# Kernel tuning notes

Hardware: AMD Instinct MI355X
Metric: run time of the kernel (lower is better)

The kernel has to match this reference:

```python
import jax, jax.numpy as jnp
import numpy as np

L, H, NH, NKV, HD, I, V, B, S = 18, 640, 4, 1, 256, 2048, 32768, 1, 1024
WINDOW = 512
EPS = 1e-6
THETA_G = 1000000.0
THETA_L = 10000.0


def _rms(x, w):
    # Gemma RMSNorm: x / rms(x) * (1 + w)
    var = jnp.mean(jnp.square(x), axis=-1, keepdims=True)
    return x * jax.lax.rsqrt(var + EPS) * (1.0 + w)


def _rope_tables(theta):
    inv = 1.0 / (theta ** (jnp.arange(0, HD, 2, dtype=jnp.float32) / HD))
    f = jnp.arange(S, dtype=jnp.float32)[:, None] * inv[None, :]
    emb = jnp.concatenate([f, f], axis=-1)  # [S, HD]
    return jnp.cos(emb), jnp.sin(emb)


def _rope(x, cos, sin):
    # x: [B, S, n, HD]
    x1, x2 = jnp.split(x, 2, axis=-1)
    rot = jnp.concatenate([-x2, x1], axis=-1)
    return x * cos[None, :, None, :] + rot * sin[None, :, None, :]


def setup_inputs() -> dict:
    key = jax.random.key(0)
    ks = jax.random.split(key, 16)
    r = lambda k, sh: jax.random.normal(k, sh, jnp.float32) * 0.02
    return {
        'input_ids': jax.random.randint(ks[0], (B, S), 0, V, jnp.int32),
        'is_full': jnp.array([(i + 1) % 6 == 0 for i in range(L)]),
        'embed': r(ks[1], (V, H)),
        'wq': r(ks[2], (L, H, NH * HD)),
        'wk': r(ks[3], (L, H, NKV * HD)),
        'wv': r(ks[4], (L, H, NKV * HD)),
        'wo': r(ks[5], (L, NH * HD, H)),
        'qn': jnp.zeros((L, HD)), 'kn': jnp.zeros((L, HD)),
        'ln1': jnp.zeros((L, H)), 'ln2': jnp.zeros((L, H)),
        'ln3': jnp.zeros((L, H)), 'ln4': jnp.zeros((L, H)),
        'wg': r(ks[6], (L, H, I)), 'wu': r(ks[7], (L, H, I)),
        'wd': r(ks[8], (L, I, H)),
        'norm_w': jnp.zeros((H,)),
    }


def _forward(embed, wq, wk, wv, wo, qn, kn, ln1, ln2, ln3, ln4, wg, wu, wd,
             norm_w, input_ids, is_full):
    cos_g, sin_g = _rope_tables(THETA_G)
    cos_l, sin_l = _rope_tables(THETA_L)
    pos = jnp.arange(S)
    causal = pos[:, None] >= pos[None, :]
    sliding = causal & ((pos[:, None] - pos[None, :]) < WINDOW)
    scale = HD ** -0.5
    grp = NH // NKV

    h = embed[input_ids] * jnp.asarray(H ** 0.5, embed.dtype)  # [B,S,H]

    def body(h, xs):
        (wq_, wk_, wv_, wo_, qn_, kn_, l1, l2, l3, l4, wg_, wu_, wd_, full) = xs
        cos = jnp.where(full, cos_g, cos_l)
        sin = jnp.where(full, sin_g, sin_l)
        mask = jnp.where(full, causal, sliding)
        x = _rms(h, l1)
        q = (x @ wq_).reshape(B, S, NH, HD)
        k = (x @ wk_).reshape(B, S, NKV, HD)
        v = (x @ wv_).reshape(B, S, NKV, HD)
        q = _rope(_rms(q, qn_), cos, sin)
        k = _rope(_rms(k, kn_), cos, sin)
        qg = q.reshape(B, S, NKV, grp, HD)
        scores = jnp.einsum('bqngd,bsnd->bngqs', qg, k) * scale
        scores = jnp.where(mask[None, None, None], scores, -1e30)
        attn = jax.nn.softmax(scores, axis=-1)
        o = jnp.einsum('bngqs,bsnd->bqngd', attn, v).reshape(B, S, NH * HD)
        h = h + _rms(o @ wo_, l2)               # post_attention_layernorm then residual
        x = _rms(h, l3)                          # pre_feedforward_layernorm
        mlp = (jax.nn.gelu(x @ wg_, approximate=True) * (x @ wu_)) @ wd_  # GeGLU
        h = h + _rms(mlp, l4)                    # post_feedforward_layernorm then residual
        return h, None

    h, _ = jax.lax.scan(body, h, (wq, wk, wv, wo, qn, kn, ln1, ln2, ln3, ln4, wg, wu, wd, is_full))
    h = _rms(h, norm_w)
    # lm_head tied to embed_tokens; final_logit_softcapping = 0.0 (disabled)
    return jnp.einsum('bsh,vh->bsv', h, embed)


def reference(input_ids, is_full, embed, wq, wk, wv, wo, qn, kn,
              ln1, ln2, ln3, ln4, wg, wu, wd, norm_w):
    return _forward(embed, wq, wk, wv, wo, qn, kn, ln1, ln2, ln3, ln4,
                    wg, wu, wd, norm_w, input_ids, is_full)
```

## Files before the change

kernel.cpp:

```cpp
#include <hip/hip_runtime.h>


typedef unsigned short u16;
typedef __attribute__((ext_vector_type(4))) float f32x4;
typedef __attribute__((ext_vector_type(8))) short bf16x8;

#define DEV static __device__ __forceinline__

DEV u16 f2bf(float f) {
  union { float f; unsigned u; } x; x.f = f;
  unsigned r = x.u + 0x7fffu + ((x.u >> 16) & 1u);
  return (u16)(r >> 16);
}

#define GLOAD16(gp, lp) __builtin_amdgcn_global_load_lds( \
    (const __attribute__((address_space(1))) void*)(gp), \
    (__attribute__((address_space(3))) void*)(lp), 16, 0, 0)

DEV float blockSum(float v, float* red) {
#pragma unroll
  for (int o = 32; o; o >>= 1) v += __shfl_down(v, o);
  int lane = threadIdx.x & 63, wid = threadIdx.x >> 6;
  if (lane == 0) red[wid] = v;
  __syncthreads();
  float s = red[0] + red[1] + red[2] + red[3];
  __syncthreads();
  return s;
}

DEV float blockMax(float v, float* red) {
#pragma unroll
  for (int o = 32; o; o >>= 1) v = fmaxf(v, __shfl_down(v, o));
  int lane = threadIdx.x & 63, wid = threadIdx.x >> 6;
  if (lane == 0) red[wid] = v;
  __syncthreads();
  float s = fmaxf(fmaxf(red[0], red[1]), fmaxf(red[2], red[3]));
  __syncthreads();
  return s;
}

DEV void cstore(float* C, size_t i, float v) { C[i] = v; }
DEV void cstore(u16* C, size_t i, float v) { C[i] = f2bf(v); }

template <typename CT, int GEGLU>
__global__ __launch_bounds__(256) void gemm_nt(
    const u16* __restrict__ A, int lda, long sA,
    const u16* __restrict__ B, int ldb, long sB,
    CT* __restrict__ C, int ldc, long sC,
    int K, float alpha, int kmode, int nshift, int ksplit) {
  __shared__ __align__(16) u16 As[2 * 128 * 64];
  __shared__ __align__(16) u16 Bs[2 * 128 * 64];
  const int m0 = blockIdx.y * 128;
  int n0;
  if (nshift == -1) n0 = blockIdx.x * 128;
  else if (nshift == -2) { n0 = blockIdx.x * 128; if (n0 > m0) return; }
  else { n0 = m0 - nshift + blockIdx.x * 128; if (n0 < 0) return; }
  int klo = 0, khi = K;
  if (kmode == 1) { klo = m0 - 512; if (klo < 0) klo = 0; khi = m0 + 128; if (khi > K) khi = K; }
  else if (kmode == 2) { khi = m0 + 128; if (khi > K) khi = K; }
  else if (kmode == 3) { int kl = K / ksplit; klo = blockIdx.z * kl; khi = klo + kl; }
  A += (long)blockIdx.z * sA;
  B += (long)blockIdx.z * sB;

  const int t = threadIdx.x;
  const int l = t & 63, w = t >> 6;
  const int wr = w >> 1, wc = w & 1;
  const int lr = l & 15, lk = l >> 4;
  const int axr = lr & 7;
  const int srow = t >> 3;
  const int scolx = ((t & 7) ^ (srow & 7)) << 3;
  const u16* Ag = A + (size_t)(m0 + srow) * lda + scolx;
  const u16* Bg = B + (size_t)(n0 + srow) * ldb + scolx;
  const int nsteps = (khi - klo) >> 6;

  auto stage = [&](int db, int k0) {
    const u16* a = Ag + k0;
    const u16* b = Bg + k0;
    u16* al = As + db * 8192 + w * 512;
    u16* bl = Bs + db * 8192 + w * 512;
#pragma unroll
    for (int p = 0; p < 4; ++p) {
      GLOAD16(a + (size_t)(32 * p) * lda, al + p * 2048);
      GLOAD16(b + (size_t)(32 * p) * ldb, bl + p * 2048);
    }
  };

  stage(0, klo);
  f32x4 acc[4][4] = {};

  for (int s = 0; s < nsteps; ++s) {
    __syncthreads();
    const int db = s & 1;
    if (s + 1 < nsteps) stage(db ^ 1, klo + (s + 1) * 64);
    const u16* Ab = As + db * 8192;
    const u16* Bb = Bs + db * 8192;
    bf16x8 af[2][4], bfr[2][4];
#pragma unroll
    for (int kk = 0; kk < 2; ++kk)
#pragma unroll
      for (int i = 0; i < 4; ++i) {
        af[kk][i]  = *(const bf16x8*)&Ab[(wr * 64 + i * 16 + lr) * 64 + (((kk * 4 + lk) ^ axr) << 3)];
        bfr[kk][i] = *(const bf16x8*)&Bb[(wc * 64 + i * 16 + lr) * 64 + (((kk * 4 + lk) ^ axr) << 3)];
      }
#pragma unroll
    for (int kk = 0; kk < 2; ++kk)
#pragma unroll
      for (int mi = 0; mi < 4; ++mi)
#pragma unroll
        for (int ni = 0; ni < 4; ++ni)
          acc[mi][ni] = __builtin_amdgcn_mfma_f32_16x16x32_bf16(af[kk][mi], bfr[kk][ni], acc[mi][ni], 0, 0, 0);
  }

  C += (long)blockIdx.z * sC;
  if (GEGLU) {
#pragma unroll
    for (int mi = 0; mi < 4; ++mi) {
      int row = m0 + wr * 64 + mi * 16 + lk * 4;
#pragma unroll
      for (int np = 0; np < 2; ++np) {
        int col = (n0 + wc * 64) / 2 + np * 16 + lr;
#pragma unroll
        for (int j = 0; j < 4; ++j) {
          float g = acc[mi][2 * np][j], u = acc[mi][2 * np + 1][j];
          float z = 0.7978845608028654f * (g + 0.044715f * g * g * g);
          float th = 2.0f / (1.0f + __expf(-2.0f * z)) - 1.0f;
          cstore(C, (size_t)(row + j) * ldc + col, 0.5f * g * (1.0f + th) * u);
        }
      }
    }
  } else {
#pragma unroll
    for (int mi = 0; mi < 4; ++mi) {
      int row = m0 + wr * 64 + mi * 16 + lk * 4;
#pragma unroll
      for (int ni = 0; ni < 4; ++ni) {
        int col = n0 + wc * 64 + ni * 16 + lr;
#pragma unroll
        for (int j = 0; j < 4; ++j)
          cstore(C, (size_t)(row + j) * ldc + col, acc[mi][ni][j] * alpha);
      }
    }
  }
}

__global__ void conv_bf16_kernel(const float* __restrict__ in, u16* __restrict__ out, long n4) {
  for (long i = (long)blockIdx.x * blockDim.x + threadIdx.x; i < n4; i += (long)gridDim.x * blockDim.x) {
    float4 v = ((const float4*)in)[i];
    ushort4 o4 = { f2bf(v.x), f2bf(v.y), f2bf(v.z), f2bf(v.w) };
    ((ushort4*)out)[i] = o4;
  }
}

__global__ void gather_rms_kernel(const int* __restrict__ ids, const float* __restrict__ embed,
                                  const float* __restrict__ w, float* __restrict__ h,
                                  u16* __restrict__ x) {
  __shared__ float red[8];
  const int s = blockIdx.x, t = threadIdx.x;
  const float* src = embed + (size_t)ids[s] * 640;
  const float scale = sqrtf(640.0f);
  float hv[3];
  float ss = 0.0f;
#pragma unroll
  for (int i = 0; i < 3; ++i) {
    int c = t + i * 256;
    float v = (c < 640) ? src[c] * scale : 0.0f;
    hv[i] = v; ss += v * v;
  }
  ss = blockSum(ss, red);
  const float sc = rsqrtf(ss * (1.0f / 640.0f) + 1e-6f);
#pragma unroll
  for (int i = 0; i < 3; ++i) {
    int c = t + i * 256;
    if (c < 640) {
      h[(size_t)s * 640 + c] = hv[i];
      x[(size_t)s * 640 + c] = f2bf(hv[i] * sc * (1.0f + w[c]));
    }
  }
}

__global__ void rms_to_bf16(const float* __restrict__ in, const float* __restrict__ w,
                            u16* __restrict__ out, int n) {
  __shared__ float red[8];
  int row = blockIdx.x;
  const float* x = in + (size_t)row * n;
  float ss = 0.0f;
  for (int c = threadIdx.x; c < n; c += blockDim.x) { float v = x[c]; ss += v * v; }
  ss = blockSum(ss, red);
  float sc = rsqrtf(ss / (float)n + 1e-6f);
  for (int c = threadIdx.x; c < n; c += blockDim.x)
    out[(size_t)row * n + c] = f2bf(x[c] * sc * (1.0f + w[c]));
}

__global__ void fused_add_norm(float* __restrict__ h, const float* __restrict__ t1,
                               int nsl, const float* __restrict__ wa,
                               const float* __restrict__ wn, u16* __restrict__ xout) {
  __shared__ float red[8];
  const int row = blockIdx.x, t = threadIdx.x;
  float ts[3], hv[3];
  float ss = 0.0f;
#pragma unroll
  for (int i = 0; i < 3; ++i) {
    int c = t + i * 256;
    float v = 0.0f;
    if (c < 640) {
      v = t1[(size_t)row * 640 + c];
      for (int z = 1; z < nsl; ++z) v += t1[(size_t)z * 655360 + (size_t)row * 640 + c];
    }
    ts[i] = v; ss += v * v;
  }
  ss = blockSum(ss, red);
  const float s1 = rsqrtf(ss * (1.0f / 640.0f) + 1e-6f);
  float ss2 = 0.0f;
#pragma unroll
  for (int i = 0; i < 3; ++i) {
    int c = t + i * 256;
    float v = 0.0f;
    if (c < 640) v = h[(size_t)row * 640 + c] + ts[i] * s1 * (1.0f + wa[c]);
    hv[i] = v; ss2 += v * v;
  }
  ss2 = blockSum(ss2, red);
  const float s2 = rsqrtf(ss2 * (1.0f / 640.0f) + 1e-6f);
#pragma unroll
  for (int i = 0; i < 3; ++i) {
    int c = t + i * 256;
    if (c < 640) {
      h[(size_t)row * 640 + c] = hv[i];
      xout[(size_t)row * 640 + c] = f2bf(hv[i] * s2 * (1.0f + wn[c]));
    }
  }
}

__global__ void rope_tables_kernel(float* cg, float* sg, float* cl, float* sl) {
  int s = blockIdx.x, t = threadIdx.x;
  float e = -(float)t * (1.0f / 128.0f);
  float ag = (float)s * expf(e * logf(1000000.0f));
  float al = (float)s * expf(e * logf(10000.0f));
  cg[s * 128 + t] = cosf(ag); sg[s * 128 + t] = sinf(ag);
  cl[s * 128 + t] = cosf(al); sl[s * 128 + t] = sinf(al);
}

__global__ void rope_fused(const float* __restrict__ qkvf, const float* __restrict__ qn,
                           const float* __restrict__ kn, u16* __restrict__ qb,
                           u16* __restrict__ kb, u16* __restrict__ vt,
                           const float* __restrict__ ct, const float* __restrict__ st) {
  __shared__ float red[8];
  __shared__ float sh[256];
  const int s = blockIdx.x, hh = blockIdx.y, t = threadIdx.x;
  if (hh == 5) {
    vt[(size_t)t * 1024 + s] = f2bf(qkvf[(size_t)s * 1536 + 1280 + t]);
    return;
  }
  const float* src = qkvf + (size_t)s * 1536 + hh * 256;
  const float* nw = (hh == 4) ? kn : qn;
  float x = src[t];
  float ss = blockSum(x * x, red);
  float n = x * rsqrtf(ss * (1.0f / 256.0f) + 1e-6f) * (1.0f + nw[t]);
  sh[t] = n;
  __syncthreads();
  float cosv = ct[s * 128 + (t & 127)];
  float sinv = st[s * 128 + (t & 127)];
  float partner = (t < 128) ? -sh[t + 128] : sh[t - 128];
  u16 r = f2bf(n * cosv + partner * sinv);
  if (hh == 4) kb[(size_t)s * 256 + t] = r;
  else qb[((size_t)hh * 1024 + s) * 256 + t] = r;
}

__global__ void softmax_kernel(const float* __restrict__ sc, u16* __restrict__ P, int mode) {
  __shared__ float red[8];
  const int i = blockIdx.x, hh = blockIdx.y, t = threadIdx.x;
  const float* row = sc + ((size_t)hh * 1024 + i) * 1024;
  u16* prow = P + ((size_t)hh * 1024 + i) * 1024;
  const int m0 = i & ~127;
  int lo = 0, wlo = 0;
  if (mode) {
    lo = i - 511; if (lo < 0) lo = 0;
    wlo = m0 - 512; if (wlo < 0) wlo = 0;
  }
  const int whi = m0 + 127;
  float m = -1e30f;
  for (int j = lo + t; j <= i; j += 256) m = fmaxf(m, row[j]);
  m = blockMax(m, red);
  float sum = 0.0f;
  for (int j = lo + t; j <= i; j += 256) sum += __expf(row[j] - m);
  sum = blockSum(sum, red);
  float inv = 1.0f / sum;
  for (int j = wlo + t; j <= whi; j += 256) {
    float v = (j >= lo && j <= i) ? __expf(row[j] - m) * inv : 0.0f;
    prow[j] = f2bf(v);
  }
}

__global__ void transpose7_kernel(
    const float* s0, const float* s1, const float* s2, const float* s3,
    const float* s4, const float* s5, const float* s6,
    u16* d0, u16* d1, u16* d2, u16* d3, u16* d45, u16* d6) {
  __shared__ float tile[64][65];
  const int ly = blockIdx.y;
  int b = blockIdx.x;
  const float* src; u16* dst; int K, N, idx, ilv = 0;
  if (b < 160)       { src = s0 + (size_t)ly * 655360;  dst = d0 + (size_t)ly * 983040;  K = 640;  N = 1024; idx = b; }
  else if (b < 200)  { src = s1 + (size_t)ly * 163840;  dst = d1 + (size_t)ly * 983040;  K = 640;  N = 256;  idx = b - 160; }
  else if (b < 240)  { src = s2 + (size_t)ly * 163840;  dst = d2 + (size_t)ly * 983040;  K = 640;  N = 256;  idx = b - 200; }
  else if (b < 400)  { src = s3 + (size_t)ly * 655360;  dst = d3 + (size_t)ly * 655360;  K = 1024; N = 640;  idx = b - 240; }
  else if (b < 720)  { src = s4 + (size_t)ly * 1310720; dst = d45 + (size_t)ly * 2621440; K = 640; N = 2048; idx = b - 400;  ilv = 1; }
  else if (b < 1040) { src = s5 + (size_t)ly * 1310720; dst = d45 + (size_t)ly * 2621440; K = 640; N = 2048; idx = b - 720;  ilv = 2; }
  else               { src = s6 + (size_t)ly * 1310720; dst = d6 + (size_t)ly * 1310720; K = 2048; N = 640; idx = b - 1040; }
  int tn = N >> 6;
  int kt = idx / tn, nt = idx % tn;
  int t = threadIdx.x;
  int lr = t >> 4, lc = (t & 15) * 4;
#pragma unroll
  for (int i = 0; i < 4; ++i) {
    float4 v = *(const float4*)&src[(size_t)(kt * 64 + lr + i * 16) * N + nt * 64 + lc];
    tile[lr + i * 16][lc] = v.x; tile[lr + i * 16][lc + 1] = v.y;
    tile[lr + i * 16][lc + 2] = v.z; tile[lr + i * 16][lc + 3] = v.w;
  }
  __syncthreads();
  int wn = t >> 3, wk8 = (t & 7) * 8;
#pragma unroll
  for (int i = 0; i < 2; ++i) {
    int gcol = nt * 64 + wn + i * 32;
    int drow = ilv ? ((gcol >> 4) * 32 + ((ilv == 2) ? 16 : 0) + (gcol & 15)) : gcol;
    u16 tmp[8];
#pragma unroll
    for (int j = 0; j < 8; ++j) tmp[j] = f2bf(tile[wk8 + j][wn + i * 32]);
    *(int4*)&dst[(size_t)drow * K + kt * 64 + wk8] = *(int4*)tmp;
  }
}

extern "C" void kernel_launch(void* const* d_in, const int* in_sizes, int n_in,
                              void* d_out, int out_size, void* d_ws, size_t ws_size,
                              hipStream_t stream) {
  (void)in_sizes; (void)n_in; (void)out_size;
  const int*   ids   = (const int*)d_in[0];
  const float* embed = (const float*)d_in[2];
  const float* wq    = (const float*)d_in[3];
  const float* wk    = (const float*)d_in[4];
  const float* wv    = (const float*)d_in[5];
  const float* wo    = (const float*)d_in[6];
  const float* qn    = (const float*)d_in[7];
  const float* kn    = (const float*)d_in[8];
  const float* ln1   = (const float*)d_in[9];
  const float* ln2   = (const float*)d_in[10];
  const float* ln3   = (const float*)d_in[11];
  const float* ln4   = (const float*)d_in[12];
  const float* wg    = (const float*)d_in[13];
  const float* wu    = (const float*)d_in[14];
  const float* wd    = (const float*)d_in[15];
  const float* nw    = (const float*)d_in[16];
  float* out = (float*)d_out;

  const int S = 1024, H = 640, NH = 4, HD = 256, I = 2048, V = 32768;

  const bool batched = ws_size >= (size_t)310 * 1024 * 1024;
  const int NL = batched ? 18 : 1;

  unsigned char* p = (unsigned char*)d_ws;
  auto alloc = [&](size_t b) { void* r = (void*)p; p += (b + 255) & ~(size_t)255; return r; };
  u16*   wqkvT = (u16*)alloc((size_t)NL * 1536 * 640 * 2);
  u16*   woT   = (u16*)alloc((size_t)NL * 640 * 1024 * 2);
  u16*   wguT  = (u16*)alloc((size_t)NL * 4096 * 640 * 2);
  u16*   wdT   = (u16*)alloc((size_t)NL * 640 * 2048 * 2);
  u16*   embT  = (u16*)alloc((size_t)V * H * 2);
  float* h     = (float*)alloc((size_t)S * H * 4);
  u16*   x     = (u16*)alloc((size_t)S * H * 2);
  float* qkvf  = (float*)alloc((size_t)S * 1536 * 4);
  u16*   qb    = (u16*)alloc((size_t)NH * S * HD * 2);
  u16*   kb    = (u16*)alloc((size_t)S * HD * 2);
  u16*   vt    = (u16*)alloc((size_t)HD * S * 2);
  float* scp   = (float*)alloc((size_t)NH * S * S * 4);
  u16*   P     = (u16*)alloc((size_t)NH * S * S * 2);
  u16*   o     = (u16*)alloc((size_t)S * NH * HD * 2);
  float* t1    = (float*)alloc((size_t)4 * S * H * 4);
  u16*   mg    = (u16*)alloc((size_t)S * I * 2);
  u16*   hn    = (u16*)alloc((size_t)S * H * 2);
  float* cg    = (float*)alloc((size_t)S * 128 * 4);
  float* sg    = (float*)alloc((size_t)S * 128 * 4);
  float* cl    = (float*)alloc((size_t)S * 128 * 4);
  float* sl2   = (float*)alloc((size_t)S * 128 * 4);

  rope_tables_kernel<<<S, 128, 0, stream>>>(cg, sg, cl, sl2);
  conv_bf16_kernel<<<2048, 256, 0, stream>>>(embed, embT, (long)V * H / 4);
  gather_rms_kernel<<<S, 256, 0, stream>>>(ids, embed, ln1, h, x);

  if (batched)
    transpose7_kernel<<<dim3(1360, 18), 256, 0, stream>>>(
        wq, wk, wv, wo, wg, wu, wd,
        wqkvT, wqkvT + (size_t)1024 * 640, wqkvT + (size_t)1280 * 640, woT, wguT, wdT);

  for (int l = 0; l < 18; ++l) {
    bool full = ((l + 1) % 6) == 0;
    size_t lw = batched ? (size_t)l : 0;
    u16* wqkvTl = wqkvT + lw * 1536 * 640;
    u16* woTl   = woT   + lw * 640 * 1024;
    u16* wguTl  = wguT  + lw * 4096 * 640;
    u16* wdTl   = wdT   + lw * 640 * 2048;

    if (!batched)
      transpose7_kernel<<<dim3(1360, 1), 256, 0, stream>>>(
          wq + (size_t)l * H * 1024, wk + (size_t)l * H * 256, wv + (size_t)l * H * 256,
          wo + (size_t)l * 1024 * H, wg + (size_t)l * H * I, wu + (size_t)l * H * I,
          wd + (size_t)l * I * H,
          wqkvTl, wqkvTl + (size_t)1024 * 640, wqkvTl + (size_t)1280 * 640, woTl, wguTl, wdTl);

    gemm_nt<float, 0><<<dim3(12, 8, 1), 256, 0, stream>>>(
        x, H, 0, wqkvTl, H, 0, qkvf, 1536, 0, H, 1.0f, 0, -1, 1);
    rope_fused<<<dim3(S, 6), 256, 0, stream>>>(qkvf, qn + l * HD, kn + l * HD, qb, kb, vt,
                                               full ? cg : cl, full ? sg : sl2);
    if (full)
      gemm_nt<float, 0><<<dim3(8, 8, NH), 256, 0, stream>>>(
          qb, HD, (long)S * HD, kb, HD, 0, scp, S, (long)S * S, HD, 0.0625f, 0, -2, 1);
    else
      gemm_nt<float, 0><<<dim3(5, 8, NH), 256, 0, stream>>>(
          qb, HD, (long)S * HD, kb, HD, 0, scp, S, (long)S * S, HD, 0.0625f, 0, 512, 1);
    softmax_kernel<<<dim3(S, NH), 256, 0, stream>>>(scp, P, full ? 0 : 1);
    gemm_nt<u16, 0><<<dim3(2, 8, NH), 256, 0, stream>>>(
        P, S, (long)S * S, vt, S, 0, o, NH * HD, HD, S, 1.0f, full ? 2 : 1, -1, 1);
    gemm_nt<float, 0><<<dim3(5, 8, 2), 256, 0, stream>>>(
        o, NH * HD, 0, woTl, NH * HD, 0, t1, H, (long)S * H, NH * HD, 1.0f, 3, -1, 2);
    fused_add_norm<<<S, 256, 0, stream>>>(h, t1, 2, ln2 + l * H, ln3 + l * H, x);

    gemm_nt<u16, 1><<<dim3(32, 8, 1), 256, 0, stream>>>(
        x, H, 0, wguTl, H, 0, mg, I, 0, H, 1.0f, 0, -1, 1);
    gemm_nt<float, 0><<<dim3(5, 8, 4), 256, 0, stream>>>(
        mg, I, 0, wdTl, I, 0, t1, H, (long)S * H, I, 1.0f, 3, -1, 4);
    fused_add_norm<<<S, 256, 0, stream>>>(h, t1, 4, ln4 + l * H,
                                          (l == 17) ? nw : ln1 + (l + 1) * H,
                                          (l == 17) ? hn : x);
  }

  gemm_nt<float, 0><<<dim3(V / 128, 8, 1), 256, 0, stream>>>(
      hn, H, 0, embT, H, 0, out, V, 0, H, 1.0f, 0, -1, 1);
}
```

Before: 2.201 ms.

## Fuse fp32 weight conversion and transposition into GEMM B-operand loads

Drops the separate weight transpose/convert and embedding-conversion kernels. The GEMM now reads fp32 weights directly from their original layout, converts them to bf16 in registers and writes them swizzled into LDS (register-staged, not async LDS loads). The QKV projection is also split over K into two partial sums that rope_fused adds back together. This removes a large pre-pass over all weights and the bf16 copies, at the cost of more global bytes per GEMM tile (fp32) and a less overlapped B pipeline.

```diff
diff --git a/kernel.cpp b/kernel.cpp
--- a/kernel.cpp
+++ b/kernel.cpp
@@ -6,6 +6,7 @@
 typedef __attribute__((ext_vector_type(8))) short bf16x8;
 
 #define DEV static __device__ __forceinline__
+#define BIGN (1 << 30)
 
 DEV u16 f2bf(float f) {
   union { float f; unsigned u; } x; x.f = f;
@@ -42,10 +43,13 @@
 DEV void cstore(float* C, size_t i, float v) { C[i] = v; }
 DEV void cstore(u16* C, size_t i, float v) { C[i] = f2bf(v); }
 
-template <typename CT, int GEGLU>
+template <typename CT, int GEGLU, int BMODE>
 __global__ __launch_bounds__(256) void gemm_nt(
     const u16* __restrict__ A, int lda, long sA,
-    const u16* __restrict__ B, int ldb, long sB,
+    const void* __restrict__ B0v, int ldb0,
+    const void* __restrict__ B1v, int ldb1,
+    const void* __restrict__ B2v, int ldb2,
+    int ns1, int ns2,
     CT* __restrict__ C, int ldc, long sC,
     int K, float alpha, int kmode, int nshift, int ksplit) {
   __shared__ __align__(16) u16 As[2 * 128 * 64];
@@ -60,7 +64,6 @@
   else if (kmode == 2) { khi = m0 + 128; if (khi > K) khi = K; }
   else if (kmode == 3) { int kl = K / ksplit; klo = blockIdx.z * kl; khi = klo + kl; }
   A += (long)blockIdx.z * sA;
-  B += (long)blockIdx.z * sB;
 
   const int t = threadIdx.x;
   const int l = t & 63, w = t >> 6;
@@ -70,28 +73,79 @@
   const int srow = t >> 3;
   const int scolx = ((t & 7) ^ (srow & 7)) << 3;
   const u16* Ag = A + (size_t)(m0 + srow) * lda + scolx;
-  const u16* Bg = B + (size_t)(n0 + srow) * ldb + scolx;
   const int nsteps = (khi - klo) >> 6;
 
-  auto stage = [&](int db, int k0) {
-    const u16* a = Ag + k0;
-    const u16* b = Bg + k0;
+  auto stageA = [&](int db, int k0) {
     u16* al = As + db * 8192 + w * 512;
+#pragma unroll
+    for (int p = 0; p < 4; ++p)
+      GLOAD16(Ag + k0 + (size_t)(32 * p) * lda, al + p * 2048);
+  };
+
+  const u16* Bg16 = nullptr;
+  const float* Bp = nullptr; int bldb = 0, bcol = 0, krow0 = 0;
+  f32x4 fb[8];
+  if constexpr (BMODE == 0) {
+    Bg16 = (const u16*)B0v + (size_t)(n0 + srow) * ldb0 + scolx;
+  } else if constexpr (BMODE == 1) {
+    int rv = n0 + (l & 31) * 4;
+    if (GEGLU) {
+      int half = (rv >> 4) & 1;
+      Bp = (const float*)(half ? B1v : B0v);
+      bldb = half ? ldb1 : ldb0;
+      bcol = (rv >> 5) * 16 + (rv & 15);
+    } else if (rv >= ns2) { Bp = (const float*)B2v; bldb = ldb2; bcol = rv - ns2; }
+    else if (rv >= ns1)   { Bp = (const float*)B1v; bldb = ldb1; bcol = rv - ns1; }
+    else                  { Bp = (const float*)B0v; bldb = ldb0; bcol = rv; }
+    krow0 = w * 16 + (l >> 5) * 8;
+  } else {
+    Bp = (const float*)B0v;
+  }
+
+  auto stageB0 = [&](int db, int k0) {
     u16* bl = Bs + db * 8192 + w * 512;
 #pragma unroll
-    for (int p = 0; p < 4; ++p) {
-      GLOAD16(a + (size_t)(32 * p) * lda, al + p * 2048);
-      GLOAD16(b + (size_t)(32 * p) * ldb, bl + p * 2048);
-    }
+    for (int p = 0; p < 4; ++p)
+      GLOAD16(Bg16 + k0 + (size_t)(32 * p) * ldb0, bl + p * 2048);
   };
-
-  stage(0, klo);
+  auto loadB = [&](int k0) {
+    if constexpr (BMODE == 1) {
+#pragma unroll
+      for (int j = 0; j < 8; ++j)
+        fb[j] = *(const f32x4*)&Bp[(size_t)(k0 + krow0 + j) * bldb + bcol];
+    } else if constexpr (BMODE == 2) {
+#pragma unroll
+      for (int p = 0; p < 4; ++p)
+#pragma unroll
+        for (int q = 0; q < 2; ++q)
+          fb[p * 2 + q] = *(const f32x4*)&Bp[(size_t)(n0 + srow + 32 * p) * ldb0 +
+                                             k0 + (((t & 7) ^ (srow & 7)) << 3) + q * 4];
+    }
+  };
+  auto writeB = [&](int db) {
+    if constexpr (BMODE == 1) {
+      int kb = w * 2 + (l >> 5);
+#pragma unroll
+      for (int e = 0; e < 4; ++e) {
+        int row = (l & 31) * 4 + e;
+        u16 tmp[8];
+#pragma unroll
+        for (int j = 0; j < 8; ++j) tmp[j] = f2bf(fb[j][e]);
+        *(int4*)&Bs[db * 8192 + row * 64 + ((kb ^ (row & 7)) << 3)] = *(int4*)tmp;
+      }
+    } else if constexpr (BMODE == 2) {
+#pragma unroll
+      for (int p = 0; p < 4; ++p) {
+        u16 tmp[8];
+#pragma unroll
+        for (int j = 0; j < 8; ++j) tmp[j] = f2bf(fb[p * 2 + j / 4][j & 3]);
+        *(int4*)&Bs[db * 8192 + (srow + 32 * p) * 64 + ((t & 7) << 3)] = *(int4*)tmp;
+      }
+    }
+  };
+
   f32x4 acc[4][4] = {};
-
-  for (int s = 0; s < nsteps; ++s) {
-    __syncthreads();
-    const int db = s & 1;
-    if (s + 1 < nsteps) stage(db ^ 1, klo + (s + 1) * 64);
+  auto compute = [&](int db) {
     const u16* Ab = As + db * 8192;
     const u16* Bb = Bs + db * 8192;
     bf16x8 af[2][4], bfr[2][4];
@@ -109,6 +163,26 @@
 #pragma unroll
         for (int ni = 0; ni < 4; ++ni)
           acc[mi][ni] = __builtin_amdgcn_mfma_f32_16x16x32_bf16(af[kk][mi], bfr[kk][ni], acc[mi][ni], 0, 0, 0);
+  };
+
+  if constexpr (BMODE == 0) {
+    stageA(0, klo); stageB0(0, klo);
+    for (int s = 0; s < nsteps; ++s) {
+      __syncthreads();
+      const int db = s & 1;
+      if (s + 1 < nsteps) { stageA(db ^ 1, klo + (s + 1) * 64); stageB0(db ^ 1, klo + (s + 1) * 64); }
+      compute(db);
+    }
+  } else {
+    loadB(klo); stageA(0, klo);
+    for (int s = 0; s < nsteps; ++s) {
+      const int db = s & 1;
+      writeB(db);
+      if (s + 1 < nsteps) loadB(klo + (s + 1) * 64);
+      __syncthreads();
+      if (s + 1 < nsteps) stageA(db ^ 1, klo + (s + 1) * 64);
+      compute(db);
+    }
   }
 
   C += (long)blockIdx.z * sC;
@@ -140,14 +214,6 @@
           cstore(C, (size_t)(row + j) * ldc + col, acc[mi][ni][j] * alpha);
       }
     }
-  }
-}
-
-__global__ void conv_bf16_kernel(const float* __restrict__ in, u16* __restrict__ out, long n4) {
-  for (long i = (long)blockIdx.x * blockDim.x + threadIdx.x; i < n4; i += (long)gridDim.x * blockDim.x) {
-    float4 v = ((const float4*)in)[i];
-    ushort4 o4 = { f2bf(v.x), f2bf(v.y), f2bf(v.z), f2bf(v.w) };
-    ((ushort4*)out)[i] = o4;
   }
 }
 
@@ -178,19 +244,6 @@
   }
 }
 
-__global__ void rms_to_bf16(const float* __restrict__ in, const float* __restrict__ w,
-                            u16* __restrict__ out, int n) {
-  __shared__ float red[8];
-  int row = blockIdx.x;
-  const float* x = in + (size_t)row * n;
-  float ss = 0.0f;
-  for (int c = threadIdx.x; c < n; c += blockDim.x) { float v = x[c]; ss += v * v; }
-  ss = blockSum(ss, red);
-  float sc = rsqrtf(ss / (float)n + 1e-6f);
-  for (int c = threadIdx.x; c < n; c += blockDim.x)
-    out[(size_t)row * n + c] = f2bf(x[c] * sc * (1.0f + w[c]));
-}
-
 __global__ void fused_add_norm(float* __restrict__ h, const float* __restrict__ t1,
                                int nsl, const float* __restrict__ wa,
                                const float* __restrict__ wn, u16* __restrict__ xout) {
@@ -246,13 +299,15 @@
   __shared__ float red[8];
   __shared__ float sh[256];
   const int s = blockIdx.x, hh = blockIdx.y, t = threadIdx.x;
+  const long SL = (long)1024 * 1536;
   if (hh == 5) {
-    vt[(size_t)t * 1024 + s] = f2bf(qkvf[(size_t)s * 1536 + 1280 + t]);
+    long i = (size_t)s * 1536 + 1280 + t;
+    vt[(size_t)t * 1024 + s] = f2bf(qkvf[i] + qkvf[i + SL]);
     return;
   }
-  const float* src = qkvf + (size_t)s * 1536 + hh * 256;
+  long i = (size_t)s * 1536 + hh * 256 + t;
   const float* nw = (hh == 4) ? kn : qn;
-  float x = src[t];
+  float x = qkvf[i] + qkvf[i + SL];
   float ss = blockSum(x * x, red);
   float n = x * rsqrtf(ss * (1.0f / 256.0f) + 1e-6f) * (1.0f + nw[t]);
   sh[t] = n;
@@ -290,48 +345,10 @@
   }
 }
 
-__global__ void transpose7_kernel(
-    const float* s0, const float* s1, const float* s2, const float* s3,
-    const float* s4, const float* s5, const float* s6,
-    u16* d0, u16* d1, u16* d2, u16* d3, u16* d45, u16* d6) {
-  __shared__ float tile[64][65];
-  const int ly = blockIdx.y;
-  int b = blockIdx.x;
-  const float* src; u16* dst; int K, N, idx, ilv = 0;
-  if (b < 160)       { src = s0 + (size_t)ly * 655360;  dst = d0 + (size_t)ly * 983040;  K = 640;  N = 1024; idx = b; }
-  else if (b < 200)  { src = s1 + (size_t)ly * 163840;  dst = d1 + (size_t)ly * 983040;  K = 640;  N = 256;  idx = b - 160; }
-  else if (b < 240)  { src = s2 + (size_t)ly * 163840;  dst = d2 + (size_t)ly * 983040;  K = 640;  N = 256;  idx = b - 200; }
-  else if (b < 400)  { src = s3 + (size_t)ly * 655360;  dst = d3 + (size_t)ly * 655360;  K = 1024; N = 640;  idx = b - 240; }
-  else if (b < 720)  { src = s4 + (size_t)ly * 1310720; dst = d45 + (size_t)ly * 2621440; K = 640; N = 2048; idx = b - 400;  ilv = 1; }
-  else if (b < 1040) { src = s5 + (size_t)ly * 1310720; dst = d45 + (size_t)ly * 2621440; K = 640; N = 2048; idx = b - 720;  ilv = 2; }
-  else               { src = s6 + (size_t)ly * 1310720; dst = d6 + (size_t)ly * 1310720; K = 2048; N = 640; idx = b - 1040; }
-  int tn = N >> 6;
-  int kt = idx / tn, nt = idx % tn;
-  int t = threadIdx.x;
-  int lr = t >> 4, lc = (t & 15) * 4;
-#pragma unroll
-  for (int i = 0; i < 4; ++i) {
-    float4 v = *(const float4*)&src[(size_t)(kt * 64 + lr + i * 16) * N + nt * 64 + lc];
-    tile[lr + i * 16][lc] = v.x; tile[lr + i * 16][lc + 1] = v.y;
-    tile[lr + i * 16][lc + 2] = v.z; tile[lr + i * 16][lc + 3] = v.w;
-  }
-  __syncthreads();
-  int wn = t >> 3, wk8 = (t & 7) * 8;
-#pragma unroll
-  for (int i = 0; i < 2; ++i) {
-    int gcol = nt * 64 + wn + i * 32;
-    int drow = ilv ? ((gcol >> 4) * 32 + ((ilv == 2) ? 16 : 0) + (gcol & 15)) : gcol;
-    u16 tmp[8];
-#pragma unroll
-    for (int j = 0; j < 8; ++j) tmp[j] = f2bf(tile[wk8 + j][wn + i * 32]);
-    *(int4*)&dst[(size_t)drow * K + kt * 64 + wk8] = *(int4*)tmp;
-  }
-}
-
 extern "C" void kernel_launch(void* const* d_in, const int* in_sizes, int n_in,
                               void* d_out, int out_size, void* d_ws, size_t ws_size,
                               hipStream_t stream) {
-  (void)in_sizes; (void)n_in; (void)out_size;
+  (void)in_sizes; (void)n_in; (void)out_size; (void)ws_size;
   const int*   ids   = (const int*)d_in[0];
   const float* embed = (const float*)d_in[2];
   const float* wq    = (const float*)d_in[3];
@@ -352,19 +369,11 @@
 
   const int S = 1024, H = 640, NH = 4, HD = 256, I = 2048, V = 32768;
 
-  const bool batched = ws_size >= (size_t)310 * 1024 * 1024;
-  const int NL = batched ? 18 : 1;
-
   unsigned char* p = (unsigned char*)d_ws;
   auto alloc = [&](size_t b) { void* r = (void*)p; p += (b + 255) & ~(size_t)255; return r; };
-  u16*   wqkvT = (u16*)alloc((size_t)NL * 1536 * 640 * 2);
-  u16*   woT   = (u16*)alloc((size_t)NL * 640 * 1024 * 2);
-  u16*   wguT  = (u16*)alloc((size_t)NL * 4096 * 640 * 2);
-  u16*   wdT   = (u16*)alloc((size_t)NL * 640 * 2048 * 2);
-  u16*   embT  = (u16*)alloc((size_t)V * H * 2);
   float* h     = (float*)alloc((size_t)S * H * 4);
   u16*   x     = (u16*)alloc((size_t)S * H * 2);
-  float* qkvf  = (float*)alloc((size_t)S * 1536 * 4);
+  float* qkvf  = (float*)alloc((size_t)2 * S * 1536 * 4);
   u16*   qb    = (u16*)alloc((size_t)NH * S * HD * 2);
   u16*   kb    = (u16*)alloc((size_t)S * HD * 2);
   u16*   vt    = (u16*)alloc((size_t)HD * S * 2);
@@ -380,55 +389,52 @@
   float* sl2   = (float*)alloc((size_t)S * 128 * 4);
 
   rope_tables_kernel<<<S, 128, 0, stream>>>(cg, sg, cl, sl2);
-  conv_bf16_kernel<<<2048, 256, 0, stream>>>(embed, embT, (long)V * H / 4);
   gather_rms_kernel<<<S, 256, 0, stream>>>(ids, embed, ln1, h, x);
-
-  if (batched)
-    transpose7_kernel<<<dim3(1360, 18), 256, 0, stream>>>(
-        wq, wk, wv, wo, wg, wu, wd,
-        wqkvT, wqkvT + (size_t)1024 * 640, wqkvT + (size_t)1280 * 640, woT, wguT, wdT);
 
   for (int l = 0; l < 18; ++l) {
     bool full = ((l + 1) % 6) == 0;
-    size_t lw = batched ? (size_t)l : 0;
-    u16* wqkvTl = wqkvT + lw * 1536 * 640;
-    u16* woTl   = woT   + lw * 640 * 1024;
-    u16* wguTl  = wguT  + lw * 4096 * 640;
-    u16* wdTl   = wdT   + lw * 640 * 2048;
-
-    if (!batched)
-      transpose7_kernel<<<dim3(1360, 1), 256, 0, stream>>>(
-          wq + (size_t)l * H * 1024, wk + (size_t)l * H * 256, wv + (size_t)l * H * 256,
-          wo + (size_t)l * 1024 * H, wg + (size_t)l * H * I, wu + (size_t)l * H * I,
-          wd + (size_t)l * I * H,
-          wqkvTl, wqkvTl + (size_t)1024 * 640, wqkvTl + (size_t)1280 * 640, woTl, wguTl, wdTl);
-
-    gemm_nt<float, 0><<<dim3(12, 8, 1), 256, 0, stream>>>(
-        x, H, 0, wqkvTl, H, 0, qkvf, 1536, 0, H, 1.0f, 0, -1, 1);
+    const float* wq_l = wq + (size_t)l * H * 1024;
+    const float* wk_l = wk + (size_t)l * H * 256;
+    const float* wv_l = wv + (size_t)l * H * 256;
+    const float* wo_l = wo + (size_t)l * 1024 * H;
+    const float* wg_l = wg + (size_t)l * H * I;
+    const float* wu_l = wu + (size_t)l * H * I;
+    const float* wd_l = wd + (size_t)l * I * H;
+
+    gemm_nt<float, 0, 1><<<dim3(12, 8, 2), 256, 0, stream>>>(
+        x, H, 0, wq_l, 1024, wk_l, 256, wv_l, 256, 1024, 1280,
+        qkvf, 1536, (long)S * 1536, H, 1.0f, 3, -1, 2);
     rope_fused<<<dim3(S, 6), 256, 0, stream>>>(qkvf, qn + l * HD, kn + l * HD, qb, kb, vt,
                                                full ? cg : cl, full ? sg : sl2);
     if (full)
-      gemm_nt<float, 0><<<dim3(8, 8, NH), 256, 0, stream>>>(
-          qb, HD, (long)S * HD, kb, HD, 0, scp, S, (long)S * S, HD, 0.0625f, 0, -2, 1);
+      gemm_nt<float, 0, 0><<<dim3(8, 8, NH), 256, 0, stream>>>(
+          qb, HD, (long)S * HD, kb, HD, nullptr, 0, nullptr, 0, BIGN, BIGN,
+          scp, S, (long)S * S, HD, 0.0625f, 0, -2, 1);
     else
-      gemm_nt<float, 0><<<dim3(5, 8, NH), 256, 0, stream>>>(
-          qb, HD, (long)S * HD, kb, HD, 0, scp, S, (long)S * S, HD, 0.0625f, 0, 512, 1);
+      gemm_nt<float, 0, 0><<<dim3(5, 8, NH), 256, 0, stream>>>(
+          qb, HD, (long)S * HD, kb, HD, nullptr, 0, nullptr, 0, BIGN, BIGN,
+          scp, S, (long)S * S, HD, 0.0625f, 0, 512, 1);
     softmax_kernel<<<dim3(S, NH), 256, 0, stream>>>(scp, P, full ? 0 : 1);
-    gemm_nt<u16, 0><<<dim3(2, 8, NH), 256, 0, stream>>>(
-        P, S, (long)S * S, vt, S, 0, o, NH * HD, HD, S, 1.0f, full ? 2 : 1, -1, 1);
-    gemm_nt<float, 0><<<dim3(5, 8, 2), 256, 0, stream>>>(
-        o, NH * HD, 0, woTl, NH * HD, 0, t1, H, (long)S * H, NH * HD, 1.0f, 3, -1, 2);
+    gemm_nt<u16, 0, 0><<<dim3(2, 8, NH), 256, 0, stream>>>(
+        P, S, (long)S * S, vt, S, nullptr, 0, nullptr, 0, BIGN, BIGN,
+        o, NH * HD, HD, S, 1.0f, full ? 2 : 1, -1, 1);
+    gemm_nt<float, 0, 1><<<dim3(5, 8, 2), 256, 0, stream>>>(
+        o, NH * HD, 0, wo_l, 640, nullptr, 0, nullptr, 0, BIGN, BIGN,
+        t1, H, (long)S * H, NH * HD, 1.0f, 3, -1, 2);
     fused_add_norm<<<S, 256, 0, stream>>>(h, t1, 2, ln2 + l * H, ln3 + l * H, x);
 
-    gemm_nt<u16, 1><<<dim3(32, 8, 1), 256, 0, stream>>>(
-        x, H, 0, wguTl, H, 0, mg, I, 0, H, 1.0f, 0, -1, 1);
-    gemm_nt<float, 0><<<dim3(5, 8, 4), 256, 0, stream>>>(
-        mg, I, 0, wdTl, I, 0, t1, H, (long)S * H, I, 1.0f, 3, -1, 4);
+    gemm_nt<u16, 1, 1><<<dim3(32, 8, 1), 256, 0, stream>>>(
+        x, H, 0, wg_l, 2048, wu_l, 2048, nullptr, 0, BIGN, BIGN,
+        mg, I, 0, H, 1.0f, 0, -1, 1);
+    gemm_nt<float, 0, 1><<<dim3(5, 8, 4), 256, 0, stream>>>(
+        mg, I, 0, wd_l, 640, nullptr, 0, nullptr, 0, BIGN, BIGN,
+        t1, H, (long)S * H, I, 1.0f, 3, -1, 4);
     fused_add_norm<<<S, 256, 0, stream>>>(h, t1, 4, ln4 + l * H,
                                           (l == 17) ? nw : ln1 + (l + 1) * H,
                                           (l == 17) ? hn : x);
   }
 
-  gemm_nt<float, 0><<<dim3(V / 128, 8, 1), 256, 0, stream>>>(
-      hn, H, 0, embT, H, 0, out, V, 0, H, 1.0f, 0, -1, 1);
-}
+  gemm_nt<float, 0, 2><<<dim3(V / 128, 8, 1), 256, 0, stream>>>(
+      hn, H, 0, embed, H, nullptr, 0, nullptr, 0, BIGN, BIGN,
+      out, V, 0, H, 1.0f, 0, -1, 1);
+}
```

Result: no change. 2.187 ms (-0.6%).
